# Optimization experiments

Hardware: AMD Instinct MI355X
Metric: run time of the kernel (lower is better)

The kernel has to match this reference:

```python
import jax, jax.numpy as jnp
import numpy as np

D_MODEL = 1024
NUM_HEADS = 16
MAX_LEN = 2048
D_HEAD = D_MODEL // NUM_HEADS
BATCH = 2
SEQ = 2048


def setup_inputs() -> dict:
    key = jax.random.key(0)
    ks = jax.random.split(key, 8)
    s = 1.0 / np.sqrt(D_MODEL)
    return {
        "x": jax.random.normal(ks[0], (BATCH, SEQ, D_MODEL), dtype=jnp.float32),
        "Wq": jax.random.uniform(ks[1], (D_MODEL, D_MODEL), jnp.float32, -s, s),
        "bq": jax.random.uniform(ks[2], (D_MODEL,), jnp.float32, -s, s),
        "Wk": jax.random.uniform(ks[3], (D_MODEL, D_MODEL), jnp.float32, -s, s),
        "bk": jax.random.uniform(ks[4], (D_MODEL,), jnp.float32, -s, s),
        "Wv": jax.random.uniform(ks[5], (D_MODEL, D_MODEL), jnp.float32, -s, s),
        "bv": jax.random.uniform(ks[6], (D_MODEL,), jnp.float32, -s, s),
        "Er": jax.random.normal(ks[7], (MAX_LEN, D_HEAD), dtype=jnp.float32),
    }


def _skew(QEr):
    # QEr: [B, H, S, S]  (music-transformer skew trick)
    B, H, S, _ = QEr.shape
    padded = jnp.pad(QEr, ((0, 0), (0, 0), (0, 0), (1, 0)))  # [B,H,S,S+1]
    reshaped = padded.reshape(B, H, S + 1, S)
    return reshaped[:, :, 1:, :]  # [B,H,S,S]


def reference(x, Wq, bq, Wk, bk, Wv, bv, Er):
    B, S, D = x.shape
    H, Dh = NUM_HEADS, D_HEAD
    # projections (torch Linear: x @ W.T + b)
    q = (jnp.einsum('bsd,ed->bse', x, Wq) + bq).reshape(B, S, H, Dh).transpose(0, 2, 1, 3)
    k = (jnp.einsum('bsd,ed->bse', x, Wk) + bk).reshape(B, S, H, Dh).transpose(0, 2, 1, 3)
    v = (jnp.einsum('bsd,ed->bse', x, Wv) + bv).reshape(B, S, H, Dh).transpose(0, 2, 1, 3)
    # relative position scores
    Er_slice = Er[MAX_LEN - S:, :]                    # [S, Dh]
    QEr = jnp.einsum('bhsd,td->bhst', q, Er_slice)    # [B,H,S,S]
    Srel = _skew(QEr)
    QKt = jnp.einsum('bhsd,bhtd->bhst', q, k)
    attn = (QKt + Srel) / jnp.sqrt(jnp.asarray(Dh, x.dtype))
    causal = jnp.tril(jnp.ones((S, S), dtype=bool))
    attn = jnp.where(causal[None, None], attn, -jnp.inf)
    attn = jax.nn.softmax(attn, axis=-1)
    out = jnp.einsum('bhst,bhtd->bhsd', attn, v)      # [B,H,S,Dh]
    out = out.transpose(0, 2, 1, 3).reshape(B, S, D)
    return out  # dropout is identity in eval mode
```

## Files before the change

### kernel.cpp

```cpp
#include <hip/hip_runtime.h>
#include <hip/hip_bf16.h>

constexpr int B  = 2;
constexpr int S  = 2048;
constexpr int D  = 1024;
constexpr int H  = 16;

typedef unsigned short u16t;
typedef unsigned long long u64;
typedef __attribute__((ext_vector_type(8))) short short8;
typedef __attribute__((ext_vector_type(4))) float float4v;

__device__ __forceinline__ float b2f(unsigned int u) {
    union { unsigned int i; float f; } c; c.i = u << 16; return c.f;
}
__device__ __forceinline__ u16t f2b(float f) {
    __hip_bfloat16 h = __float2bfloat16(f);
    union { __hip_bfloat16 h; u16t u; } c; c.h = h; return c.u;
}
__device__ __forceinline__ unsigned int pkbf(float a, float b) {
    return (unsigned int)f2b(a) | ((unsigned int)f2b(b) << 16);
}
__device__ __forceinline__ u64 pack4(float4 v) {
    return (u64)f2b(v.x) | ((u64)f2b(v.y) << 16) | ((u64)f2b(v.z) << 32) | ((u64)f2b(v.w) << 48);
}

typedef __attribute__((address_space(1))) const unsigned int* as1_u32p;
typedef __attribute__((address_space(3))) unsigned int* as3_u32p;
__device__ __forceinline__ void gll16(const void* g, void* l) {
    __builtin_amdgcn_global_load_lds((as1_u32p)g, (as3_u32p)l, 16, 0, 0);
}

constexpr size_t XB_OFF = 0;
constexpr size_t WQ_OFF = 4194304;
constexpr size_t WK_OFF = 5242880;
constexpr size_t WV_OFF = 6291456;
constexpr size_t ER_OFF = 7340032;
constexpr size_t QW_OFF = 7471104;
constexpr size_t KW_OFF = 11665408;
constexpr size_t VT_OFF = 15859712;

__global__ __launch_bounds__(256) void prep_bf16(
    const float* __restrict__ x,  const float* __restrict__ Wq,
    const float* __restrict__ Wk, const float* __restrict__ Wv,
    const float* __restrict__ Er, u64* __restrict__ dst)
{
    size_t i4 = (size_t)blockIdx.x * 256 + threadIdx.x;
    const float* src; size_t off;
    if      (i4 < 1048576) { src = x;  off = i4; }
    else if (i4 < 1310720) { src = Wq; off = i4 - 1048576; }
    else if (i4 < 1572864) { src = Wk; off = i4 - 1310720; }
    else if (i4 < 1835008) { src = Wv; off = i4 - 1572864; }
    else                   { src = Er; off = i4 - 1835008; }
    float4 v = ((const float4*)src)[off];
    dst[i4] = pack4(v);
}

__global__ __launch_bounds__(256, 3) void qkv_mfma(
    const u16t* __restrict__ xb,
    const u16t* __restrict__ wqb, const u16t* __restrict__ wkb, const u16t* __restrict__ wvb,
    const float* __restrict__ bq, const float* __restrict__ bk, const float* __restrict__ bv,
    u16t* __restrict__ qo, u16t* __restrict__ ko, u16t* __restrict__ vT)
{
    const int z = blockIdx.z;
    const u16t*  W    = (z == 0) ? wqb : (z == 1) ? wkb : wvb;
    const float* bias = (z == 0) ? bq  : (z == 1) ? bk  : bv;

    __shared__ __align__(16) u16t Xs[128 * 64];
    __shared__ __align__(16) u16t Ws[128 * 64];
    char* XsB = (char*)Xs;
    char* WsB = (char*)Ws;

    const int tid = threadIdx.x;
    const int w = tid >> 6, lane = tid & 63;
    const int quad = lane >> 4, l16 = lane & 15;
    const int m0 = blockIdx.x * 128, n0 = blockIdx.y * 128;
    const int mi = (w >> 1) * 64, ni = (w & 1) * 64;

    const int srow = lane >> 3;
    const int d8s  = (lane & 7) ^ (srow & 7);
    const int xk   = l16 & 7;

    float4v acc[4][4];
    #pragma unroll
    for (int mt = 0; mt < 4; ++mt)
        #pragma unroll
        for (int nt = 0; nt < 4; ++nt) acc[mt][nt] = (float4v){0.f, 0.f, 0.f, 0.f};

    for (int k0 = 0; k0 < D; k0 += 64) {
        #pragma unroll
        for (int it = 0; it < 4; ++it) {
            int ci  = w * 4 + it;
            int row = ci * 8 + srow;
            gll16(&xb[(size_t)(m0 + row) * D + k0 + d8s * 8], XsB + ci * 1024);
            gll16(&W [(size_t)(n0 + row) * D + k0 + d8s * 8], WsB + ci * 1024);
        }
        __syncthreads();

        short8 af[4][2], bf[4][2];
        #pragma unroll
        for (int mt = 0; mt < 4; ++mt) {
            int r = mi + mt * 16 + l16;
            af[mt][0] = *(const short8*)(XsB + r * 128 + ((quad       ^ xk) << 4));
            af[mt][1] = *(const short8*)(XsB + r * 128 + (((quad + 4) ^ xk) << 4));
        }
        #pragma unroll
        for (int nt = 0; nt < 4; ++nt) {
            int r = ni + nt * 16 + l16;
            bf[nt][0] = *(const short8*)(WsB + r * 128 + ((quad       ^ xk) << 4));
            bf[nt][1] = *(const short8*)(WsB + r * 128 + (((quad + 4) ^ xk) << 4));
        }
        #pragma unroll
        for (int mt = 0; mt < 4; ++mt)
            #pragma unroll
            for (int nt = 0; nt < 4; ++nt) {
                acc[mt][nt] = __builtin_amdgcn_mfma_f32_16x16x32_bf16(af[mt][0], bf[nt][0], acc[mt][nt], 0, 0, 0);
                acc[mt][nt] = __builtin_amdgcn_mfma_f32_16x16x32_bf16(af[mt][1], bf[nt][1], acc[mt][nt], 0, 0, 0);
            }
        __syncthreads();
    }

    float bias_v[4];
    #pragma unroll
    for (int nt = 0; nt < 4; ++nt) bias_v[nt] = bias[n0 + ni + nt * 16 + l16];

    #pragma unroll
    for (int mt = 0; mt < 4; ++mt)
        #pragma unroll
        for (int nt = 0; nt < 4; ++nt) {
            int n = n0 + ni + nt * 16 + l16;
            int h = n >> 6, dh = n & 63;
            int mb = m0 + mi + mt * 16 + quad * 4;
            int b_ = mb >> 11, s = mb & (S - 1);
            if (z == 2) {
                float4 o;
                o.x = acc[mt][nt][0] + bias_v[nt];
                o.y = acc[mt][nt][1] + bias_v[nt];
                o.z = acc[mt][nt][2] + bias_v[nt];
                o.w = acc[mt][nt][3] + bias_v[nt];
                *(u64*)&vT[((size_t)(b_ * H + h) * 64 + dh) * S + s] = pack4(o);
            } else {
                u16t* out = (z == 0) ? qo : ko;
                #pragma unroll
                for (int rg = 0; rg < 4; ++rg)
                    out[((size_t)(b_ * H + h) * S + s + rg) * 64 + dh] =
                        f2b(acc[mt][nt][rg] + bias_v[nt]);
            }
        }
}

__global__ __launch_bounds__(256, 4) void attn_mfma(
    const u16t* __restrict__ q, const u16t* __restrict__ k,
    const u16t* __restrict__ vT, const u16t* __restrict__ er,
    float* __restrict__ out)
{
    __shared__ __align__(16) u16t KsS[2][64 * 64];
    __shared__ __align__(16) u16t VsS[2][64 * 64];
    __shared__ __align__(16) u16t PsS[64 * 64];
    char* KsB = (char*)KsS;
    char* VsB = (char*)VsS;
    char* PsB = (char*)PsS;
    float* lrows = (float*)PsS;

    const int tid = threadIdx.x;
    const int w = tid >> 6, lane = tid & 63;
    const int quad = lane >> 4, l16 = lane & 15;

    const int r_  = blockIdx.x;
    const int g   = blockIdx.y;
    const int bh  = r_ & 31;
    const int slot = r_ >> 5;
    const int ix  = (g == 0) ? (31 - slot)
                  : (g == 1) ? (16 + slot)
                  : (g == 2) ? (15 - slot)
                  :            slot;
    const int hh = bh & (H - 1), bb = bh >> 4;

    const u16t* qb = q  + (size_t)bh * S * 64;
    const u16t* kb = k  + (size_t)bh * S * 64;
    const u16t* vb = vT + (size_t)bh * 64 * S;

    const int xk = (l16 & 7);
    const float SC = 0.18033688f;
    const float M2 = 17.3125f;

    const int srow = lane >> 3;
    const int d8s  = (lane & 7) ^ (srow & 7);

    const int s0 = ix * 64;

    const size_t qoff = (size_t)(s0 + w * 16 + l16) * 64;
    const short8 Qa0 = *(const short8*)&qb[qoff + quad * 8];
    const short8 Qa1 = *(const short8*)&qb[qoff + 32 + quad * 8];

    float4v accO[4], L[5];
    #pragma unroll
    for (int t = 0; t < 4; ++t) accO[t] = (float4v){0.f, 0.f, 0.f, 0.f};
    float lsum[4] = {0.f, 0.f, 0.f, 0.f};

    #pragma unroll
    for (int it = 0; it < 2; ++it) {
        int ci = w * 2 + it;
        int prow = ci * 8 + srow;
        gll16(&kb[(size_t)prow * 64 + d8s * 8], KsB + ci * 1024);
        gll16(&vb[(size_t)prow * S + d8s * 8], VsB + ci * 1024);
    }
    __syncthreads();

    for (int jt = 0; jt <= ix; ++jt) {
        const int t0 = jt * 64;
        const int jbase = S - 64 - s0 + t0;
        const bool diag = (jt == ix);
        const int bsel = (jt & 1) * 8192;

        short8 ef0[4], ef1[4], e00, e01;
        #pragma unroll
        for (int c = 1; c <= 4; ++c) {
            int grow = jbase + (3 - w + c) * 16 + l16;
            if (grow > S - 1) grow = S - 1;
            const u16t* ep = &er[(size_t)grow * 64 + quad * 8];
            ef0[c - 1] = *(const short8*)ep;
            ef1[c - 1] = *(const short8*)(ep + 32);
        }
        if (jt == 0) {
            int grow = jbase + (3 - w) * 16 + l16;
            if (grow > S - 1) grow = S - 1;
            const u16t* ep = &er[(size_t)grow * 64 + quad * 8];
            e00 = *(const short8*)ep;
            e01 = *(const short8*)(ep + 32);
        }

        if (jt < ix) {
            int nb = ((jt + 1) & 1) * 8192;
            #pragma unroll
            for (int it = 0; it < 2; ++it) {
                int ci = w * 2 + it;
                int prow = ci * 8 + srow;
                gll16(&kb[(size_t)(t0 + 64 + prow) * 64 + d8s * 8], KsB + nb + ci * 1024);
                gll16(&vb[(size_t)prow * S + t0 + 64 + d8s * 8], VsB + nb + ci * 1024);
            }
        }

        float4v S1[4];
        #pragma unroll
        for (int nt = 0; nt < 4; ++nt) {
            int row = nt * 16 + l16;
            short8 b0 = *(const short8*)(KsB + bsel + row * 128 + ((quad ^ xk) << 4));
            short8 b1 = *(const short8*)(KsB + bsel + row * 128 + (((quad + 4) ^ xk) << 4));
            float4v a = (float4v){0.f, 0.f, 0.f, 0.f};
            a = __builtin_amdgcn_mfma_f32_16x16x32_bf16(Qa0, b0, a, 0, 0, 0);
            a = __builtin_amdgcn_mfma_f32_16x16x32_bf16(Qa1, b1, a, 0, 0, 0);
            S1[nt] = a;
        }

        if (jt == 0) {
            float4v e = (float4v){0.f, 0.f, 0.f, 0.f};
            e = __builtin_amdgcn_mfma_f32_16x16x32_bf16(Qa0, e00, e, 0, 0, 0);
            e = __builtin_amdgcn_mfma_f32_16x16x32_bf16(Qa1, e01, e, 0, 0, 0);
            L[0] = e;
        } else {
            L[0] = L[4];
        }
        #pragma unroll
        for (int c = 1; c <= 4; ++c) {
            float4v e = (float4v){0.f, 0.f, 0.f, 0.f};
            e = __builtin_amdgcn_mfma_f32_16x16x32_bf16(Qa0, ef0[c - 1], e, 0, 0, 0);
            e = __builtin_amdgcn_mfma_f32_16x16x32_bf16(Qa1, ef1[c - 1], e, 0, 0, 0);
            L[c] = e;
        }

        #pragma unroll
        for (int rg = 0; rg < 4; ++rg) {
            const int usel = quad * 4 + rg;
            const int thr = 15 - usel;
            const int sidx = ((lane & 48) | ((l16 + thr) & 15)) * 4;
            const bool give_lo = (l16 >= thr);
            unsigned int p01 = give_lo ? pkbf(L[0][rg], L[1][rg]) : pkbf(L[1][rg], L[2][rg]);
            unsigned int p23 = give_lo ? pkbf(L[2][rg], L[3][rg]) : pkbf(L[3][rg], L[4][rg]);
            unsigned int q01 = (unsigned int)__builtin_amdgcn_ds_bpermute(sidx, (int)p01);
            unsigned int q23 = (unsigned int)__builtin_amdgcn_ds_bpermute(sidx, (int)p23);
            float qe[4] = { b2f(q01 & 0xffffu), b2f(q01 >> 16),
                            b2f(q23 & 0xffffu), b2f(q23 >> 16) };
            const int i_ = w * 16 + usel;
            const int ikey = i_ & 7;
            float psum = 0.f;
            #pragma unroll
            for (int nt = 0; nt < 4; ++nt) {
                float s2 = fmaf(S1[nt][rg] + qe[nt], SC, -M2);
                float p = (diag && (nt * 16 + l16 > i_)) ? 0.f : exp2f(s2);
                psum += p;
                int j_ = nt * 16 + l16;
                *(u16t*)(PsB + i_ * 128 + (((j_ >> 3) ^ ikey) << 4) + (j_ & 7) * 2) = f2b(p);
            }
            lsum[rg] += psum;
        }

        {
            int ar = w * 16 + l16;
            short8 pa0 = *(const short8*)(PsB + ar * 128 + ((quad ^ (ar & 7)) << 4));
            short8 pa1 = *(const short8*)(PsB + ar * 128 + (((quad + 4) ^ (ar & 7)) << 4));
            #pragma unroll
            for (int td = 0; td < 4; ++td) {
                int row = td * 16 + l16;
                short8 a0 = *(const short8*)(VsB + bsel + row * 128 + ((quad ^ xk) << 4));
                short8 a1 = *(const short8*)(VsB + bsel + row * 128 + (((quad + 4) ^ xk) << 4));
                accO[td] = __builtin_amdgcn_mfma_f32_16x16x32_bf16(a0, pa0, accO[td], 0, 0, 0);
                accO[td] = __builtin_amdgcn_mfma_f32_16x16x32_bf16(a1, pa1, accO[td], 0, 0, 0);
            }
        }
        __syncthreads();
    }

    #pragma unroll
    for (int rg = 0; rg < 4; ++rg) {
        float s = lsum[rg];
        s += __shfl_xor(s, 1);
        s += __shfl_xor(s, 2);
        s += __shfl_xor(s, 4);
        s += __shfl_xor(s, 8);
        if (l16 == 0) lrows[w * 16 + quad * 4 + rg] = s;
    }
    float inv = 1.f / lrows[w * 16 + l16];

    float* ob = out + (size_t)bb * S * D + (size_t)hh * 64
                + (size_t)(s0 + w * 16 + l16) * D;
    #pragma unroll
    for (int td = 0; td < 4; ++td) {
        float4 o;
        o.x = accO[td][0] * inv;
        o.y = accO[td][1] * inv;
        o.z = accO[td][2] * inv;
        o.w = accO[td][3] * inv;
        *(float4*)&ob[td * 16 + quad * 4] = o;
    }
}

extern "C" void kernel_launch(void* const* d_in, const int* in_sizes, int n_in,
                              void* d_out, int out_size, void* d_ws, size_t ws_size,
                              hipStream_t stream) {
    const float* x  = (const float*)d_in[0];
    const float* Wq = (const float*)d_in[1];
    const float* bq = (const float*)d_in[2];
    const float* Wk = (const float*)d_in[3];
    const float* bk = (const float*)d_in[4];
    const float* Wv = (const float*)d_in[5];
    const float* bv = (const float*)d_in[6];
    const float* Er = (const float*)d_in[7];
    float* out = (float*)d_out;

    u16t* ws16 = (u16t*)d_ws;
    u16t* xb  = ws16 + XB_OFF;
    u16t* wqb = ws16 + WQ_OFF;
    u16t* wkb = ws16 + WK_OFF;
    u16t* wvb = ws16 + WV_OFF;
    u16t* erb = ws16 + ER_OFF;
    u16t* qw  = ws16 + QW_OFF;
    u16t* kw  = ws16 + KW_OFF;
    u16t* vTw = ws16 + VT_OFF;

    prep_bf16<<<dim3(7296), dim3(256), 0, stream>>>(x, Wq, Wk, Wv, Er, (u64*)d_ws);

    qkv_mfma<<<dim3(32, 8, 3), dim3(256), 0, stream>>>(
        xb, wqb, wkb, wvb, bq, bk, bv, qw, kw, vTw);

    attn_mfma<<<dim3(256, 4), dim3(256), 0, stream>>>(qw, kw, vTw, erb, out);
}
```

Before: 200.5 us.

## Stage QKV epilogue through LDS for coalesced stores, tweak attention softmax

The QKV projection epilogue now adds bias in registers, writes the tile into padded shared memory one head-half at a time, and then emits 16-byte coalesced global stores for q/k and for the transposed v, replacing scattered 2-byte and 8-byte stores. In the attention kernel, the skewed relative-position values are exchanged as full fp32 via four bpermutes instead of two packed bf16 ones. The softmax body is specialised for diagonal and off-diagonal tiles, and s_setprio is raised around the MFMA sections. This adds extra barriers and LDS traffic in the projection epilogue and more permute instructions in the attention loop.

```diff
diff --git a/kernel.cpp b/kernel.cpp
--- a/kernel.cpp
+++ b/kernel.cpp
@@ -18,8 +18,11 @@
     __hip_bfloat16 h = __float2bfloat16(f);
     union { __hip_bfloat16 h; u16t u; } c; c.h = h; return c.u;
 }
-__device__ __forceinline__ unsigned int pkbf(float a, float b) {
-    return (unsigned int)f2b(a) | ((unsigned int)f2b(b) << 16);
+__device__ __forceinline__ int fasi(float f) {
+    union { float f; int i; } c; c.f = f; return c.i;
+}
+__device__ __forceinline__ float iasf(int i) {
+    union { int i; float f; } c; c.i = i; return c.f;
 }
 __device__ __forceinline__ u64 pack4(float4 v) {
     return (u64)f2b(v.x) | ((u64)f2b(v.y) << 16) | ((u64)f2b(v.z) << 32) | ((u64)f2b(v.w) << 48);
@@ -66,10 +69,9 @@
     const u16t*  W    = (z == 0) ? wqb : (z == 1) ? wkb : wvb;
     const float* bias = (z == 0) ? bq  : (z == 1) ? bk  : bv;
 
-    __shared__ __align__(16) u16t Xs[128 * 64];
-    __shared__ __align__(16) u16t Ws[128 * 64];
-    char* XsB = (char*)Xs;
-    char* WsB = (char*)Ws;
+    __shared__ __align__(16) u16t SMEM[2 * 128 * 64];
+    char* XsB = (char*)SMEM;
+    char* WsB = XsB + 16384;
 
     const int tid = threadIdx.x;
     const int w = tid >> 6, lane = tid & 63;
@@ -123,30 +125,72 @@
     float bias_v[4];
     #pragma unroll
     for (int nt = 0; nt < 4; ++nt) bias_v[nt] = bias[n0 + ni + nt * 16 + l16];
-
     #pragma unroll
     for (int mt = 0; mt < 4; ++mt)
         #pragma unroll
-        for (int nt = 0; nt < 4; ++nt) {
-            int n = n0 + ni + nt * 16 + l16;
-            int h = n >> 6, dh = n & 63;
-            int mb = m0 + mi + mt * 16 + quad * 4;
-            int b_ = mb >> 11, s = mb & (S - 1);
-            if (z == 2) {
-                float4 o;
-                o.x = acc[mt][nt][0] + bias_v[nt];
-                o.y = acc[mt][nt][1] + bias_v[nt];
-                o.z = acc[mt][nt][2] + bias_v[nt];
-                o.w = acc[mt][nt][3] + bias_v[nt];
-                *(u64*)&vT[((size_t)(b_ * H + h) * 64 + dh) * S + s] = pack4(o);
-            } else {
-                u16t* out = (z == 0) ? qo : ko;
+        for (int nt = 0; nt < 4; ++nt)
+            #pragma unroll
+            for (int rg = 0; rg < 4; ++rg) acc[mt][nt][rg] += bias_v[nt];
+
+    const int hB = n0 >> 6;
+    const int b_ = m0 >> 11;
+    const int sB = m0 & (S - 1);
+    char* EP = (char*)SMEM;
+
+    if (z < 2) {
+        u16t* outp = (z == 0) ? qo : ko;
+        #pragma unroll 1
+        for (int hp = 0; hp < 2; ++hp) {
+            __syncthreads();
+            if ((w & 1) == hp) {
                 #pragma unroll
-                for (int rg = 0; rg < 4; ++rg)
-                    out[((size_t)(b_ * H + h) * S + s + rg) * 64 + dh] =
-                        f2b(acc[mt][nt][rg] + bias_v[nt]);
-            }
-        }
+                for (int mt = 0; mt < 4; ++mt)
+                    #pragma unroll
+                    for (int nt = 0; nt < 4; ++nt) {
+                        int col = nt * 16 + l16;
+                        #pragma unroll
+                        for (int rg = 0; rg < 4; ++rg) {
+                            int row = mi + mt * 16 + quad * 4 + rg;
+                            *(u16t*)(EP + row * 144 + col * 2) = f2b(acc[mt][nt][rg]);
+                        }
+                    }
+            }
+            __syncthreads();
+            #pragma unroll
+            for (int it = 0; it < 4; ++it) {
+                int idx = tid + it * 256;
+                int row = idx >> 3, c8 = idx & 7;
+                short8 vv = *(const short8*)(EP + row * 144 + c8 * 16);
+                *(short8*)&outp[((size_t)(b_ * H + hB + hp) * S + sB + row) * 64 + c8 * 8] = vv;
+            }
+        }
+    } else {
+        #pragma unroll 1
+        for (int hp = 0; hp < 2; ++hp) {
+            __syncthreads();
+            if ((w & 1) == hp) {
+                #pragma unroll
+                for (int mt = 0; mt < 4; ++mt)
+                    #pragma unroll
+                    for (int nt = 0; nt < 4; ++nt) {
+                        int rowD = nt * 16 + l16;
+                        #pragma unroll
+                        for (int rg = 0; rg < 4; ++rg) {
+                            int colS = mi + mt * 16 + quad * 4 + rg;
+                            *(u16t*)(EP + rowD * 272 + colS * 2) = f2b(acc[mt][nt][rg]);
+                        }
+                    }
+            }
+            __syncthreads();
+            #pragma unroll
+            for (int it = 0; it < 4; ++it) {
+                int idx = tid + it * 256;
+                int rowD = idx >> 4, c16 = idx & 15;
+                short8 vv = *(const short8*)(EP + rowD * 272 + c16 * 16);
+                *(short8*)&vT[((size_t)(b_ * H + hB + hp) * 64 + rowD) * S + sB + c16 * 8] = vv;
+            }
+        }
+    }
 }
 
 __global__ __launch_bounds__(256, 4) void attn_mfma(
@@ -241,6 +285,7 @@
             }
         }
 
+        __builtin_amdgcn_s_setprio(1);
         float4v S1[4];
         #pragma unroll
         for (int nt = 0; nt < 4; ++nt) {
@@ -268,34 +313,39 @@
             e = __builtin_amdgcn_mfma_f32_16x16x32_bf16(Qa1, ef1[c - 1], e, 0, 0, 0);
             L[c] = e;
         }
-
-        #pragma unroll
-        for (int rg = 0; rg < 4; ++rg) {
-            const int usel = quad * 4 + rg;
-            const int thr = 15 - usel;
-            const int sidx = ((lane & 48) | ((l16 + thr) & 15)) * 4;
-            const bool give_lo = (l16 >= thr);
-            unsigned int p01 = give_lo ? pkbf(L[0][rg], L[1][rg]) : pkbf(L[1][rg], L[2][rg]);
-            unsigned int p23 = give_lo ? pkbf(L[2][rg], L[3][rg]) : pkbf(L[3][rg], L[4][rg]);
-            unsigned int q01 = (unsigned int)__builtin_amdgcn_ds_bpermute(sidx, (int)p01);
-            unsigned int q23 = (unsigned int)__builtin_amdgcn_ds_bpermute(sidx, (int)p23);
-            float qe[4] = { b2f(q01 & 0xffffu), b2f(q01 >> 16),
-                            b2f(q23 & 0xffffu), b2f(q23 >> 16) };
-            const int i_ = w * 16 + usel;
-            const int ikey = i_ & 7;
-            float psum = 0.f;
-            #pragma unroll
-            for (int nt = 0; nt < 4; ++nt) {
-                float s2 = fmaf(S1[nt][rg] + qe[nt], SC, -M2);
-                float p = (diag && (nt * 16 + l16 > i_)) ? 0.f : exp2f(s2);
-                psum += p;
-                int j_ = nt * 16 + l16;
-                *(u16t*)(PsB + i_ * 128 + (((j_ >> 3) ^ ikey) << 4) + (j_ & 7) * 2) = f2b(p);
-            }
-            lsum[rg] += psum;
-        }
+        __builtin_amdgcn_s_setprio(0);
+
+#define SM_BODY(DIAGC)                                                        \
+        _Pragma("unroll")                                                     \
+        for (int rg = 0; rg < 4; ++rg) {                                      \
+            const int usel = quad * 4 + rg;                                   \
+            const int thr = 15 - usel;                                        \
+            const int sidx = ((lane & 48) | ((l16 + thr) & 15)) * 4;          \
+            const bool give_lo = (l16 >= thr);                                \
+            int t0v = __builtin_amdgcn_ds_bpermute(sidx, fasi(give_lo ? L[0][rg] : L[1][rg])); \
+            int t1v = __builtin_amdgcn_ds_bpermute(sidx, fasi(give_lo ? L[1][rg] : L[2][rg])); \
+            int t2v = __builtin_amdgcn_ds_bpermute(sidx, fasi(give_lo ? L[2][rg] : L[3][rg])); \
+            int t3v = __builtin_amdgcn_ds_bpermute(sidx, fasi(give_lo ? L[3][rg] : L[4][rg])); \
+            float qe[4] = { iasf(t0v), iasf(t1v), iasf(t2v), iasf(t3v) };     \
+            const int i_ = w * 16 + usel;                                     \
+            const int ikey = i_ & 7;                                          \
+            float psum = 0.f;                                                 \
+            _Pragma("unroll")                                                 \
+            for (int nt = 0; nt < 4; ++nt) {                                  \
+                float s2 = fmaf(S1[nt][rg] + qe[nt], SC, -M2);                \
+                float p = exp2f(s2);                                          \
+                if (DIAGC) p = (nt * 16 + l16 > i_) ? 0.f : p;                \
+                psum += p;                                                    \
+                int j_ = nt * 16 + l16;                                       \
+                *(u16t*)(PsB + i_ * 128 + (((j_ >> 3) ^ ikey) << 4) + (j_ & 7) * 2) = f2b(p); \
+            }                                                                 \
+            lsum[rg] += psum;                                                 \
+        }
+        if (diag) { SM_BODY(true) } else { SM_BODY(false) }
+#undef SM_BODY
 
         {
+            __builtin_amdgcn_s_setprio(1);
             int ar = w * 16 + l16;
             short8 pa0 = *(const short8*)(PsB + ar * 128 + ((quad ^ (ar & 7)) << 4));
             short8 pa1 = *(const short8*)(PsB + ar * 128 + (((quad + 4) ^ (ar & 7)) << 4));
@@ -307,6 +357,7 @@
                 accO[td] = __builtin_amdgcn_mfma_f32_16x16x32_bf16(a0, pa0, accO[td], 0, 0, 0);
                 accO[td] = __builtin_amdgcn_mfma_f32_16x16x32_bf16(a1, pa1, accO[td], 0, 0, 0);
             }
+            __builtin_amdgcn_s_setprio(0);
         }
         __syncthreads();
     }
```

After: 214.0 us. 1.07x slower.
